# Optimization experiments

Hardware: AMD Instinct MI355X
Metric: run time of the kernel (lower is better)

Reference implementation:

```python
import jax, jax.numpy as jnp
import numpy as np

N = 20000
E = 320000
NEG_SLOPE = 0.2
LN_EPS = 1e-5


def gat_conv(x, W, a_src, a_dst, b, src, dst, heads, ch, concat):
    # x: [N, F_in]; W: [F_in, H*C]; a_src/a_dst: [H, C]; b: [H*C] or [C]
    xl = (x @ W).reshape(N, heads, ch)                      # [N,H,C]
    alpha_src = jnp.sum(xl * a_src, axis=-1)                # [N,H]
    alpha_dst = jnp.sum(xl * a_dst, axis=-1)                # [N,H]
    e = alpha_src[src] + alpha_dst[dst]                     # [E',H]
    e = jax.nn.leaky_relu(e, NEG_SLOPE)
    # segment softmax over incoming edges of each dst node
    m = jax.ops.segment_max(e, dst, num_segments=N)         # [N,H]
    m = jnp.where(jnp.isfinite(m), m, 0.0)
    ex = jnp.exp(e - m[dst])
    denom = jax.ops.segment_sum(ex, dst, num_segments=N)    # [N,H]
    alpha = ex / (denom[dst] + 1e-16)                       # [E',H]
    msg = alpha[:, :, None] * xl[src]                       # [E',H,C]
    out = jax.ops.segment_sum(msg, dst, num_segments=N)     # [N,H,C]
    if concat:
        return out.reshape(N, heads * ch) + b
    return out.mean(axis=1) + b


def layer_norm(x, g, b):
    mu = jnp.mean(x, axis=-1, keepdims=True)
    var = jnp.mean(jnp.square(x - mu), axis=-1, keepdims=True)
    return (x - mu) * jax.lax.rsqrt(var + LN_EPS) * g + b


def setup_inputs() -> dict:
    key = jax.random.key(0)
    ks = jax.random.split(key, 24)
    d = {}
    d["x"] = jax.random.normal(ks[0], (N, 50), dtype=jnp.float32)
    d["edge_index"] = jax.random.randint(ks[1], (2, E), 0, N, dtype=jnp.int64)

    def glorot(k, shape):
        fan = shape[0] + shape[-1]
        return jax.random.normal(k, shape, dtype=jnp.float32) * np.sqrt(2.0 / fan)

    # conv1: 50 -> 256, heads=4, concat
    d["W1"] = glorot(ks[2], (50, 4 * 256))
    d["a_src1"] = glorot(ks[3], (4, 256))
    d["a_dst1"] = glorot(ks[4], (4, 256))
    d["b1"] = jnp.zeros((4 * 256,), jnp.float32)
    # conv2: 1024 -> 256, heads=4, concat
    d["W2"] = glorot(ks[5], (1024, 4 * 256))
    d["a_src2"] = glorot(ks[6], (4, 256))
    d["a_dst2"] = glorot(ks[7], (4, 256))
    d["b2"] = jnp.zeros((4 * 256,), jnp.float32)
    # conv3: 1024 -> 121, heads=6, concat=False
    d["W3"] = glorot(ks[8], (1024, 6 * 121))
    d["a_src3"] = glorot(ks[9], (6, 121))
    d["a_dst3"] = glorot(ks[10], (6, 121))
    d["b3"] = jnp.zeros((121,), jnp.float32)
    # skips
    d["skipW1"] = glorot(ks[11], (50, 1024))
    d["skipb1"] = jnp.zeros((1024,), jnp.float32)
    d["skipW2"] = glorot(ks[12], (1024, 1024))
    d["skipb2"] = jnp.zeros((1024,), jnp.float32)
    # layer norms
    d["g1"] = jnp.ones((1024,), jnp.float32)
    d["beta1"] = jnp.zeros((1024,), jnp.float32)
    d["g2"] = jnp.ones((1024,), jnp.float32)
    d["beta2"] = jnp.zeros((1024,), jnp.float32)
    return d


def reference(x, edge_index, W1, a_src1, a_dst1, b1, W2, a_src2, a_dst2, b2,
              W3, a_src3, a_dst3, b3, skipW1, skipb1, skipW2, skipb2,
              g1, beta1, g2, beta2):
    # add self loops (PyG GATConv default)
    loop = jnp.arange(N, dtype=edge_index.dtype)
    src = jnp.concatenate([edge_index[0], loop])
    dst = jnp.concatenate([edge_index[1], loop])

    h = gat_conv(x, W1, a_src1, a_dst1, b1, src, dst, 4, 256, True)
    h = jax.nn.elu(layer_norm(h + (x @ skipW1 + skipb1), g1, beta1))
    h2 = gat_conv(h, W2, a_src2, a_dst2, b2, src, dst, 4, 256, True)
    h2 = jax.nn.elu(layer_norm(h2 + (h @ skipW2 + skipb2), g2, beta2))
    out = gat_conv(h2, W3, a_src3, a_dst3, b3, src, dst, 6, 121, False)
    return out
```

## Files before the change

### kernel.cpp

```cpp
#include <hip/hip_runtime.h>
#include <hip/hip_bf16.h>
#include <math.h>

typedef _Float16 h16;
typedef __attribute__((ext_vector_type(8))) _Float16 h16x8;
typedef __attribute__((ext_vector_type(4))) float f32x4;

#if __has_builtin(__builtin_amdgcn_global_load_lds)
#define GLD16(g, l)                                                                      \
    __builtin_amdgcn_global_load_lds(                                                    \
        (const __attribute__((address_space(1))) unsigned int*)(g),                      \
        (__attribute__((address_space(3))) unsigned int*)(l), 16, 0, 0)
#else
#define GLD16(g, l) (*(f32x4*)(l) = *(const f32x4*)(g))
#endif

#define GEMM_BODY(A, Bt, K, STORE)                                                       \
    __shared__ h16 As[128 * 32];                                                         \
    __shared__ h16 Bs[128 * 32];                                                         \
    const int t = threadIdx.x;                                                           \
    const int lane = t & 63;                                                             \
    const int wid = t >> 6;                                                              \
    const int wm = (wid >> 1) << 6;                                                      \
    const int wn = (wid & 1) << 6;                                                       \
    const int bm = blockIdx.y * 128;                                                     \
    const int bn = blockIdx.x * 128;                                                     \
    const int srow = (wid << 4) + (lane >> 2);                                           \
    const int scol = (lane & 3) << 3;                                                    \
    const h16* pa0 = A + (size_t)(bm + srow) * K + scol;                                 \
    const h16* pa1 = A + (size_t)(bm + 64 + srow) * K + scol;                            \
    const h16* pb0 = Bt + (size_t)(bn + srow) * K + scol;                                \
    const h16* pb1 = Bt + (size_t)(bn + 64 + srow) * K + scol;                           \
    h16* la0 = As + srow * 32 + scol;                                                    \
    h16* la1 = As + (64 + srow) * 32 + scol;                                             \
    h16* lb0 = Bs + srow * 32 + scol;                                                    \
    h16* lb1 = Bs + (64 + srow) * 32 + scol;                                             \
    f32x4 acc[4][4];                                                                     \
    _Pragma("unroll") for (int i = 0; i < 4; i++)                                        \
        _Pragma("unroll") for (int j = 0; j < 4; j++)                                    \
            acc[i][j] = (f32x4){0.f, 0.f, 0.f, 0.f};                                     \
    const int m16 = lane & 15;                                                           \
    const int k8 = (lane >> 4) << 3;                                                     \
    for (int k0 = 0; k0 < K; k0 += 32) {                                                 \
        __syncthreads();                                                                 \
        GLD16(pa0, la0);                                                                 \
        GLD16(pa1, la1);                                                                 \
        GLD16(pb0, lb0);                                                                 \
        GLD16(pb1, lb1);                                                                 \
        pa0 += 32; pa1 += 32; pb0 += 32; pb1 += 32;                                      \
        __syncthreads();                                                                 \
        h16x8 af[4], bfr[4];                                                             \
        _Pragma("unroll") for (int i = 0; i < 4; i++) {                                  \
            af[i] = *(const h16x8*)(As + (wm + 16 * i + m16) * 32 + k8);                 \
            bfr[i] = *(const h16x8*)(Bs + (wn + 16 * i + m16) * 32 + k8);                \
        }                                                                                \
        _Pragma("unroll") for (int i = 0; i < 4; i++)                                    \
            _Pragma("unroll") for (int j = 0; j < 4; j++)                                \
                acc[i][j] = __builtin_amdgcn_mfma_f32_16x16x32_f16(af[i], bfr[j],        \
                                                                   acc[i][j], 0, 0, 0);  \
    }                                                                                    \
    const int r4 = (lane >> 4) << 2;                                                     \
    STORE

__global__ __launch_bounds__(256) void gemm_bt(const h16* __restrict__ A,
                                               const h16* __restrict__ Bt,
                                               h16* __restrict__ C,
                                               int M, int N, int K) {
    GEMM_BODY(A, Bt, K,
        _Pragma("unroll") for (int i = 0; i < 4; i++)
            _Pragma("unroll") for (int j = 0; j < 4; j++) {
                int col = bn + wn + 16 * j + m16;
                _Pragma("unroll") for (int r = 0; r < 4; r++) {
                    int row = bm + wm + 16 * i + r4 + r;
                    C[(size_t)row * N + col] = (h16)acc[i][j][r];
                }
            })
}

__global__ __launch_bounds__(256) void gemm_bt2(const h16* __restrict__ A,
                                                const h16* __restrict__ Bt,
                                                h16* __restrict__ C0,
                                                h16* __restrict__ C1,
                                                int M, int K) {
    GEMM_BODY(A, Bt, K,
        h16* Cp = (bn < 1024) ? C0 : C1;
        const int cb = bn & 1023;
        _Pragma("unroll") for (int i = 0; i < 4; i++)
            _Pragma("unroll") for (int j = 0; j < 4; j++) {
                int col = cb + wn + 16 * j + m16;
                _Pragma("unroll") for (int r = 0; r < 4; r++) {
                    int row = bm + wm + 16 * i + r4 + r;
                    Cp[(size_t)row * 1024 + col] = (h16)acc[i][j][r];
                }
            })
}

__device__ __forceinline__ void transpose_tile(const float* __restrict__ W,
                                               h16* __restrict__ WT,
                                               int K, int N, int Kp, int Np,
                                               int bx, int by, float* sm) {
    int tx = threadIdx.x & 31, ty = threadIdx.x >> 5;
#pragma unroll
    for (int r = ty; r < 32; r += 8) {
        int k = by * 32 + r, n = bx * 32 + tx;
        float v = 0.f;
        if (k < K && n < N) v = W[(size_t)k * N + n];
        sm[r * 33 + tx] = v;
    }
    __syncthreads();
#pragma unroll
    for (int r = ty; r < 32; r += 8) {
        int n = bx * 32 + r, k = by * 32 + tx;
        if (n < Np && k < Kp) WT[(size_t)n * Kp + k] = (h16)sm[tx * 33 + r];
    }
}

__device__ __forceinline__ void transpose_w3_tile(const float* __restrict__ W,
                                                  h16* __restrict__ WT,
                                                  int bx, int by, float* sm) {
    int tx = threadIdx.x & 31, ty = threadIdx.x >> 5;
    int r0 = bx * 32;
    int h = r0 >> 7;
    int c0 = r0 & 127;
#pragma unroll
    for (int r = ty; r < 32; r += 8) {
        int k = by * 32 + r;
        int c = c0 + tx;
        float v = 0.f;
        if (c < 121) v = W[(size_t)k * 726 + h * 121 + c];
        sm[r * 33 + tx] = v;
    }
    __syncthreads();
#pragma unroll
    for (int r = ty; r < 32; r += 8) {
        int rr = r0 + r;
        int k = by * 32 + tx;
        WT[(size_t)rr * 1024 + k] = (h16)sm[tx * 33 + r];
    }
}

__global__ __launch_bounds__(256) void prep_k(const float* __restrict__ x,
                                              const float* __restrict__ W1,
                                              const float* __restrict__ sW1,
                                              const float* __restrict__ W2,
                                              const float* __restrict__ sW2,
                                              const float* __restrict__ W3,
                                              h16* __restrict__ xp,
                                              h16* __restrict__ WTcat1,
                                              h16* __restrict__ WTcat2,
                                              h16* __restrict__ W3pT, int Nn) {
    __shared__ float sm[32 * 33];
    int b = blockIdx.x;
    if (b < 5024) {
        int i = b * 256 + threadIdx.x;
        int n = i >> 6, c = i & 63;
        float v = 0.f;
        if (n < Nn && c < 50) v = x[n * 50 + c];
        xp[(size_t)n * 64 + c] = (h16)v;
    } else if (b < 5088) {
        int i = b - 5024; transpose_tile(W1, WTcat1, 50, 1024, 64, 1024, i % 32, i / 32, sm);
    } else if (b < 5152) {
        int i = b - 5088; transpose_tile(sW1, WTcat1 + 1024 * 64, 50, 1024, 64, 1024, i % 32, i / 32, sm);
    } else if (b < 6176) {
        int i = b - 5152; transpose_tile(W2, WTcat2, 1024, 1024, 1024, 1024, i % 32, i / 32, sm);
    } else if (b < 7200) {
        int i = b - 6176; transpose_tile(sW2, WTcat2 + (size_t)1024 * 1024, 1024, 1024, 1024, 1024, i % 32, i / 32, sm);
    } else {
        int i = b - 7200; transpose_w3_tile(W3, W3pT, i % 24, i / 24, sm);
    }
}

__global__ void zero_probe_k(const int* __restrict__ ei, int* __restrict__ cnt,
                             int* __restrict__ flag, int Nn) {
    int i = blockIdx.x * 256 + threadIdx.x;
    if (i < Nn) cnt[i] = 0;
    if (blockIdx.x == 0 && threadIdx.x == 0) {
        int all0 = 1;
        for (int k = 0; k < 64; k++)
            if (ei[2 * k + 1] != 0) { all0 = 0; break; }
        *flag = all0;
    }
}

__device__ __forceinline__ int load_ei(const int* ei, int idx, int is64) {
    return is64 ? ei[2 * idx] : ei[idx];
}

__global__ void hist_k(const int* __restrict__ ei, const int* __restrict__ flag,
                       int* __restrict__ cnt, int E, int Nn) {
    int e = blockIdx.x * 256 + threadIdx.x;
    if (e >= E + Nn) return;
    int is64 = *flag;
    int d = (e < E) ? load_ei(ei, E + e, is64) : (e - E);
    d = min(max(d, 0), Nn - 1);
    atomicAdd(&cnt[d], 1);
}

__global__ __launch_bounds__(1024) void scan_k(int* __restrict__ cnt, int* __restrict__ row_ptr,
                                               int Nn) {
    __shared__ int part[1024];
    int t = threadIdx.x;
    int chunk = (Nn + 1023) >> 10;
    int lo = t * chunk;
    int hi = lo + chunk; if (hi > Nn) hi = Nn; if (lo > Nn) lo = Nn;
    int s = 0;
    for (int i = lo; i < hi; i++) s += (cnt[i] + 7) & ~7;
    part[t] = s;
    __syncthreads();
    for (int off = 1; off < 1024; off <<= 1) {
        int v = (t >= off) ? part[t - off] : 0;
        __syncthreads();
        part[t] += v;
        __syncthreads();
    }
    int run = part[t] - s;
    for (int i = lo; i < hi; i++) { row_ptr[i] = run; run += (cnt[i] + 7) & ~7; }
    if (t == 1023) row_ptr[Nn] = part[1023];
    __syncthreads();
    for (int i = lo; i < hi; i++) cnt[i] = 0;
}

__global__ void fill_csr_k(const int* __restrict__ ei, const int* __restrict__ flag,
                           const int* __restrict__ row_ptr, int* __restrict__ cursor,
                           int* __restrict__ src_csr, int E, int Nn) {
    int e = blockIdx.x * 256 + threadIdx.x;
    if (e >= E + Nn) return;
    int is64 = *flag;
    int d = (e < E) ? load_ei(ei, E + e, is64) : (e - E);
    int s = (e < E) ? load_ei(ei, e, is64) : (e - E);
    d = min(max(d, 0), Nn - 1);
    s = min(max(s, 0), Nn - 1);
    int slot = row_ptr[d] + atomicAdd(&cursor[d], 1);
    src_csr[slot] = s;
}

__global__ void alpha_k(const h16* __restrict__ XL, int ld, const float* __restrict__ a_src,
                        const float* __restrict__ a_dst, float* __restrict__ asrc,
                        float* __restrict__ adst, int Nn, int H, int C, int Cpad) {
    int gw = (blockIdx.x * 256 + threadIdx.x) >> 6;
    int lane = threadIdx.x & 63;
    if (gw >= Nn * H) return;
    int n = gw / H, h = gw - n * H;
    const h16* row = XL + (size_t)n * ld + h * Cpad;
    const float* as = a_src + h * C;
    const float* ad = a_dst + h * C;
    float s = 0.f, d = 0.f;
    for (int c = lane; c < C; c += 64) {
        float v = (float)row[c];
        s += v * as[c];
        d += v * ad[c];
    }
#pragma unroll
    for (int off = 32; off; off >>= 1) {
        s += __shfl_down(s, off);
        d += __shfl_down(d, off);
    }
    if (lane == 0) { asrc[n * H + h] = s; adst[n * H + h] = d; }
}

__global__ void attn_k(const int* __restrict__ row_ptr, const int* __restrict__ deg,
                       const int* __restrict__ src_csr,
                       const float* __restrict__ asrc, const float* __restrict__ adst,
                       float* __restrict__ wt, int Nn, int H, int Ecap) {
    int gw = (blockIdx.x * 256 + threadIdx.x) >> 6;
    int lane = threadIdx.x & 63;
    if (gw >= Nn) return;
    int n = gw;
    int base = row_ptr[n], dg = deg[n];
    if (dg <= 64) {
        bool v = lane < dg;
        int src = v ? src_csr[base + lane] : 0;
        for (int h = 0; h < H; h++) {
            float ad = adst[n * H + h];
            float e = -1e30f;
            if (v) {
                e = asrc[src * H + h] + ad;
                e = e > 0.f ? e : 0.2f * e;
            }
            float m = e;
#pragma unroll
            for (int off = 1; off < 64; off <<= 1) m = fmaxf(m, __shfl_xor(m, off));
            float ex = v ? __expf(e - m) : 0.f;
            float sum = ex;
#pragma unroll
            for (int off = 1; off < 64; off <<= 1) sum += __shfl_xor(sum, off);
            if (v) wt[(size_t)h * Ecap + base + lane] = ex / (sum + 1e-16f);
        }
        return;
    }
    for (int h = 0; h < H; h++) {
        float ad = adst[n * H + h];
        float m = -1e30f;
        for (int s = lane; s < dg; s += 64) {
            float e = asrc[src_csr[base + s] * H + h] + ad;
            e = e > 0.f ? e : 0.2f * e;
            m = fmaxf(m, e);
        }
#pragma unroll
        for (int off = 1; off < 64; off <<= 1) m = fmaxf(m, __shfl_xor(m, off));
        float sum = 0.f;
        for (int s = lane; s < dg; s += 64) {
            float e = asrc[src_csr[base + s] * H + h] + ad;
            e = e > 0.f ? e : 0.2f * e;
            sum += __expf(e - m);
        }
#pragma unroll
        for (int off = 1; off < 64; off <<= 1) sum += __shfl_xor(sum, off);
        float inv = 1.f / (sum + 1e-16f);
        float* wrow = wt + (size_t)h * Ecap;
        for (int s = lane; s < dg; s += 64) {
            float e = asrc[src_csr[base + s] * H + h] + ad;
            e = e > 0.f ? e : 0.2f * e;
            wrow[base + s] = __expf(e - m) * inv;
        }
    }
}

__global__ __launch_bounds__(256) void agg_skip8(const h16* __restrict__ XL,
                                                 const float* __restrict__ wt,
                                                 const int* __restrict__ row_ptr,
                                                 const int* __restrict__ src_csr,
                                                 const float* __restrict__ bias,
                                                 const float* __restrict__ sb,
                                                 h16* __restrict__ SK, int Nn, int Ecap) {
    const int cc = blockIdx.x;
    const int n = blockIdx.y * 4 + (threadIdx.x >> 6);
    const int lane = threadIdx.x & 63;
    if (n >= Nn) return;
    const int g = lane >> 4;
    const int p = lane & 15;
    const int col = cc * 128 + p * 8;
    const float* wrow = wt + (size_t)(cc >> 1) * Ecap;
    const h16* XLc = XL + col;
    const int base = row_ptr[n], end = row_ptr[n + 1];

    float acc[8];
#pragma unroll
    for (int j = 0; j < 8; j++) acc[j] = 0.f;

    for (int e = base; e < end; e += 8) {
        int2 si = *(const int2*)(src_csr + e + 2 * g);
        float2 wv = *(const float2*)(wrow + e + 2 * g);
        h16x8 xa = *(const h16x8*)(XLc + (size_t)si.x * 1024);
        h16x8 xb = *(const h16x8*)(XLc + (size_t)si.y * 1024);
#pragma unroll
        for (int j = 0; j < 8; j++) acc[j] += wv.x * (float)xa[j] + wv.y * (float)xb[j];
    }
#pragma unroll
    for (int j = 0; j < 8; j++) {
        acc[j] += __shfl_xor(acc[j], 16);
        acc[j] += __shfl_xor(acc[j], 32);
    }
    if (lane < 16) {
        size_t o = (size_t)n * 1024 + col;
        h16x8 sk = *(const h16x8*)(SK + o);
        h16x8 res;
#pragma unroll
        for (int j = 0; j < 8; j++)
            res[j] = (h16)(acc[j] + bias[col + j] + sb[col + j] + (float)sk[j]);
        *(h16x8*)(SK + o) = res;
    }
}

__global__ __launch_bounds__(256) void agg_mean8(const h16* __restrict__ XL,
                                                 const float* __restrict__ wt,
                                                 const int* __restrict__ row_ptr,
                                                 const int* __restrict__ src_csr,
                                                 h16* __restrict__ part, int Nn, int Ecap) {
    const int cc = blockIdx.x;
    const int n = blockIdx.y * 4 + (threadIdx.x >> 6);
    const int lane = threadIdx.x & 63;
    if (n >= Nn) return;
    const int g = lane >> 4;
    const int p = lane & 15;
    const int col = cc * 128 + p * 8;
    const float* wrow = wt + (size_t)cc * Ecap;
    const h16* XLc = XL + col;
    const int base = row_ptr[n], end = row_ptr[n + 1];

    float acc[8];
#pragma unroll
    for (int j = 0; j < 8; j++) acc[j] = 0.f;

    for (int e = base; e < end; e += 8) {
        int2 si = *(const int2*)(src_csr + e + 2 * g);
        float2 wv = *(const float2*)(wrow + e + 2 * g);
        h16x8 xa = *(const h16x8*)(XLc + (size_t)si.x * 768);
        h16x8 xb = *(const h16x8*)(XLc + (size_t)si.y * 768);
#pragma unroll
        for (int j = 0; j < 8; j++) acc[j] += wv.x * (float)xa[j] + wv.y * (float)xb[j];
    }
#pragma unroll
    for (int j = 0; j < 8; j++) {
        acc[j] += __shfl_xor(acc[j], 16);
        acc[j] += __shfl_xor(acc[j], 32);
    }
    if (lane < 16) {
        size_t o = (size_t)n * 768 + col;
        h16x8 res;
#pragma unroll
        for (int j = 0; j < 8; j++) res[j] = (h16)acc[j];
        *(h16x8*)(part + o) = res;
    }
}

__global__ __launch_bounds__(128) void reduce_mean_k(const h16* __restrict__ part,
                                                     const float* __restrict__ b3,
                                                     float* __restrict__ out, int Nn) {
    int n = blockIdx.x;
    int t = threadIdx.x;
    if (t >= 121) return;
    const h16* row = part + (size_t)n * 768;
    float s = 0.f;
#pragma unroll
    for (int h = 0; h < 6; h++) s += (float)row[h * 128 + t];
    out[(size_t)n * 121 + t] = s * (1.f / 6.f) + b3[t];
}

__global__ __launch_bounds__(256) void ln_elu_k(const h16* __restrict__ in,
                                                const float* __restrict__ g,
                                                const float* __restrict__ be,
                                                h16* __restrict__ out, int rows_real) {
    const int D = 1024;
    int n = blockIdx.x;
    int t = threadIdx.x;
    size_t ro = (size_t)n * D;
    if (n >= rows_real) {
#pragma unroll
        for (int j = 0; j < 4; j++) out[ro + t + 256 * j] = (h16)0.f;
        return;
    }
    float v[4];
    float s = 0.f, q = 0.f;
#pragma unroll
    for (int j = 0; j < 4; j++) {
        int c = t + 256 * j;
        float a = (float)in[ro + c];
        v[j] = a;
        s += a;
        q += a * a;
    }
#pragma unroll
    for (int off = 32; off; off >>= 1) {
        s += __shfl_down(s, off);
        q += __shfl_down(q, off);
    }
    __shared__ float rs[8];
    int wid = t >> 6;
    if ((t & 63) == 0) { rs[wid] = s; rs[wid + 4] = q; }
    __syncthreads();
    s = rs[0] + rs[1] + rs[2] + rs[3];
    q = rs[4] + rs[5] + rs[6] + rs[7];
    float mu = s * (1.f / 1024.f);
    float var = q * (1.f / 1024.f) - mu * mu;
    float inv = rsqrtf(fmaxf(var, 0.f) + 1e-5f);
#pragma unroll
    for (int j = 0; j < 4; j++) {
        int c = t + 256 * j;
        float y = (v[j] - mu) * inv * g[c] + be[c];
        y = y > 0.f ? y : expm1f(y);
        out[ro + c] = (h16)y;
    }
}

extern "C" void kernel_launch(void* const* d_in, const int* in_sizes, int n_in,
                              void* d_out, int out_size, void* d_ws, size_t ws_size,
                              hipStream_t stream) {
    const float* x   = (const float*)d_in[0];
    const int*   ei  = (const int*)d_in[1];
    const float* W1  = (const float*)d_in[2];
    const float* as1 = (const float*)d_in[3];
    const float* ad1 = (const float*)d_in[4];
    const float* b1  = (const float*)d_in[5];
    const float* W2  = (const float*)d_in[6];
    const float* as2 = (const float*)d_in[7];
    const float* ad2 = (const float*)d_in[8];
    const float* b2  = (const float*)d_in[9];
    const float* W3  = (const float*)d_in[10];
    const float* as3 = (const float*)d_in[11];
    const float* ad3 = (const float*)d_in[12];
    const float* b3  = (const float*)d_in[13];
    const float* sW1 = (const float*)d_in[14];
    const float* sb1 = (const float*)d_in[15];
    const float* sW2 = (const float*)d_in[16];
    const float* sb2 = (const float*)d_in[17];
    const float* g1  = (const float*)d_in[18];
    const float* be1 = (const float*)d_in[19];
    const float* g2  = (const float*)d_in[20];
    const float* be2 = (const float*)d_in[21];
    float* out = (float*)d_out;

    const int Nn = 20000;
    const int E = in_sizes[1] / 2;
    const int E2 = E + Nn;
    const int Ecap = E2 + 8 * Nn;
    const int Mpad = 20096;

    char* p = (char*)d_ws;
    auto alloc = [&](size_t bytes) {
        char* r = p;
        p += (bytes + 255) & ~(size_t)255;
        return r;
    };
    h16*   WTcat1 = (h16*)alloc((size_t)2048 * 64 * 2);
    h16*   WTcat2 = (h16*)alloc((size_t)2048 * 1024 * 2);
    h16*   W3pT   = (h16*)alloc((size_t)768 * 1024 * 2);
    h16*   xp     = (h16*)alloc((size_t)Mpad * 64 * 2);
    h16*   XL     = (h16*)alloc((size_t)Mpad * 1024 * 2);
    h16*   SK     = (h16*)alloc((size_t)Mpad * 1024 * 2);
    h16*   H1     = (h16*)alloc((size_t)Mpad * 1024 * 2);
    float* asrcb  = (float*)alloc((size_t)Nn * 6 * 4);
    float* adstb  = (float*)alloc((size_t)Nn * 6 * 4);
    float* wbuf   = (float*)alloc((size_t)6 * Ecap * 4);
    int*   rowp   = (int*)alloc((size_t)(Nn + 1) * 4);
    int*   cnt    = (int*)alloc((size_t)Nn * 4);
    int*   scsr   = (int*)alloc((size_t)Ecap * 4);
    int*   eiflag = (int*)alloc(256);
    h16*   part   = SK;
    (void)ws_size; (void)n_in; (void)out_size;

    prep_k<<<7968, 256, 0, stream>>>(x, W1, sW1, W2, sW2, W3, xp, WTcat1, WTcat2, W3pT, Nn);

    zero_probe_k<<<(Nn + 255) / 256, 256, 0, stream>>>(ei, cnt, eiflag, Nn);
    hist_k<<<(E2 + 255) / 256, 256, 0, stream>>>(ei, eiflag, cnt, E, Nn);
    scan_k<<<1, 1024, 0, stream>>>(cnt, rowp, Nn);
    (void)hipMemsetAsync(scsr, 0, (size_t)Ecap * 4, stream);
    (void)hipMemsetAsync(wbuf, 0, (size_t)6 * Ecap * 4, stream);
    fill_csr_k<<<(E2 + 255) / 256, 256, 0, stream>>>(ei, eiflag, rowp, cnt, scsr, E, Nn);

    gemm_bt2<<<dim3(16, Mpad / 128), 256, 0, stream>>>(xp, WTcat1, XL, SK, Mpad, 64);
    alpha_k<<<(Nn * 4 * 64) / 256, 256, 0, stream>>>(XL, 1024, as1, ad1, asrcb, adstb, Nn, 4, 256, 256);
    attn_k<<<(Nn + 3) / 4, 256, 0, stream>>>(rowp, cnt, scsr, asrcb, adstb, wbuf, Nn, 4, Ecap);
    agg_skip8<<<dim3(8, (Nn + 3) / 4), 256, 0, stream>>>(XL, wbuf, rowp, scsr, b1, sb1, SK, Nn, Ecap);
    ln_elu_k<<<Mpad, 256, 0, stream>>>(SK, g1, be1, H1, Nn);

    gemm_bt2<<<dim3(16, Mpad / 128), 256, 0, stream>>>(H1, WTcat2, XL, SK, Mpad, 1024);
    alpha_k<<<(Nn * 4 * 64) / 256, 256, 0, stream>>>(XL, 1024, as2, ad2, asrcb, adstb, Nn, 4, 256, 256);
    attn_k<<<(Nn + 3) / 4, 256, 0, stream>>>(rowp, cnt, scsr, asrcb, adstb, wbuf, Nn, 4, Ecap);
    agg_skip8<<<dim3(8, (Nn + 3) / 4), 256, 0, stream>>>(XL, wbuf, rowp, scsr, b2, sb2, SK, Nn, Ecap);
    ln_elu_k<<<Mpad, 256, 0, stream>>>(SK, g2, be2, H1, Nn);

    gemm_bt<<<dim3(6, Mpad / 128), 256, 0, stream>>>(H1, W3pT, XL, Mpad, 768, 1024);
    alpha_k<<<(Nn * 6 * 64) / 256, 256, 0, stream>>>(XL, 768, as3, ad3, asrcb, adstb, Nn, 6, 121, 128);
    attn_k<<<(Nn + 3) / 4, 256, 0, stream>>>(rowp, cnt, scsr, asrcb, adstb, wbuf, Nn, 6, Ecap);
    agg_mean8<<<dim3(6, (Nn + 3) / 4), 256, 0, stream>>>(XL, wbuf, rowp, scsr, part, Nn, Ecap);
    reduce_mean_k<<<Nn, 128, 0, stream>>>(part, b3, out, Nn);
}
```

Measured before the change: 782.4 us.

## Double GEMM K-tile to 64 with XOR-swizzled LDS and fuse zeroing kernels

The shared GEMM body now stages a 64-wide K slice per iteration instead of 32. This halves the number of barrier pairs per tile, and the LDS layout uses an XOR swizzle on 16-byte chunks to avoid bank conflicts on fragment reads. Separately, the count, CSR and weight-buffer zeroing is folded into one kernel, replacing two hipMemsetAsync calls and cutting launch overhead. The larger LDS footprint may reduce occupancy. The K=64 layer-1 GEMM now runs a single iteration.

```diff
diff --git a/kernel.cpp b/kernel.cpp
--- a/kernel.cpp
+++ b/kernel.cpp
@@ -16,8 +16,8 @@
 #endif
 
 #define GEMM_BODY(A, Bt, K, STORE)                                                       \
-    __shared__ h16 As[128 * 32];                                                         \
-    __shared__ h16 Bs[128 * 32];                                                         \
+    __shared__ h16 As[128 * 64];                                                         \
+    __shared__ h16 Bs[128 * 64];                                                         \
     const int t = threadIdx.x;                                                           \
     const int lane = t & 63;                                                             \
     const int wid = t >> 6;                                                              \
@@ -25,34 +25,50 @@
     const int wn = (wid & 1) << 6;                                                       \
     const int bm = blockIdx.y * 128;                                                     \
     const int bn = blockIdx.x * 128;                                                     \
-    const int srow = (wid << 4) + (lane >> 2);                                           \
-    const int scol = (lane & 3) << 3;                                                    \
-    const h16* pa0 = A + (size_t)(bm + srow) * K + scol;                                 \
-    const h16* pa1 = A + (size_t)(bm + 64 + srow) * K + scol;                            \
-    const h16* pb0 = Bt + (size_t)(bn + srow) * K + scol;                                \
-    const h16* pb1 = Bt + (size_t)(bn + 64 + srow) * K + scol;                           \
-    h16* la0 = As + srow * 32 + scol;                                                    \
-    h16* la1 = As + (64 + srow) * 32 + scol;                                             \
-    h16* lb0 = Bs + srow * 32 + scol;                                                    \
-    h16* lb1 = Bs + (64 + srow) * 32 + scol;                                             \
+    const int sr = (wid << 3) + (lane >> 3);                                  \
+    const int sc_dst = (lane & 7) << 3;                                                  \
+    const int sc_src = (((lane & 7) ^ (sr & 7)) << 3);                                   \
+    const h16* pa0 = A + (size_t)(bm + sr) * K + sc_src;                                 \
+    const h16* pa1 = A + (size_t)(bm + sr + 32) * K + sc_src;                            \
+    const h16* pa2 = A + (size_t)(bm + sr + 64) * K + sc_src;                            \
+    const h16* pa3 = A + (size_t)(bm + sr + 96) * K + sc_src;                            \
+    const h16* pb0 = Bt + (size_t)(bn + sr) * K + sc_src;                                \
+    const h16* pb1 = Bt + (size_t)(bn + sr + 32) * K + sc_src;                           \
+    const h16* pb2 = Bt + (size_t)(bn + sr + 64) * K + sc_src;                           \
+    const h16* pb3 = Bt + (size_t)(bn + sr + 96) * K + sc_src;                           \
+    h16* la0 = As + sr * 64 + sc_dst;                                                    \
+    h16* la1 = la0 + 32 * 64;                                                            \
+    h16* la2 = la0 + 64 * 64;                                                            \
+    h16* la3 = la0 + 96 * 64;                                                            \
+    h16* lb0 = Bs + sr * 64 + sc_dst;                                                    \
+    h16* lb1 = lb0 + 32 * 64;                                                            \
+    h16* lb2 = lb0 + 64 * 64;                                                            \
+    h16* lb3 = lb0 + 96 * 64;                                                            \
     f32x4 acc[4][4];                                                                     \
     _Pragma("unroll") for (int i = 0; i < 4; i++)                                        \
         _Pragma("unroll") for (int j = 0; j < 4; j++)                                    \
             acc[i][j] = (f32x4){0.f, 0.f, 0.f, 0.f};                                     \
     const int m16 = lane & 15;                                                           \
-    const int k8 = (lane >> 4) << 3;                                                     \
-    for (int k0 = 0; k0 < K; k0 += 32) {                                                 \
+    const int k8s = (((lane >> 4) ^ (m16 & 7)) << 3);                                    \
+    for (int k0 = 0; k0 < K; k0 += 64) {                                                 \
         __syncthreads();                                                                 \
-        GLD16(pa0, la0);                                                                 \
-        GLD16(pa1, la1);                                                                 \
-        GLD16(pb0, lb0);                                                                 \
-        GLD16(pb1, lb1);                                                                 \
-        pa0 += 32; pa1 += 32; pb0 += 32; pb1 += 32;                                      \
+        GLD16(pa0, la0); GLD16(pa1, la1); GLD16(pa2, la2); GLD16(pa3, la3);              \
+        GLD16(pb0, lb0); GLD16(pb1, lb1); GLD16(pb2, lb2); GLD16(pb3, lb3);              \
+        pa0 += 64; pa1 += 64; pa2 += 64; pa3 += 64;                                      \
+        pb0 += 64; pb1 += 64; pb2 += 64; pb3 += 64;                                      \
         __syncthreads();                                                                 \
         h16x8 af[4], bfr[4];                                                             \
         _Pragma("unroll") for (int i = 0; i < 4; i++) {                                  \
-            af[i] = *(const h16x8*)(As + (wm + 16 * i + m16) * 32 + k8);                 \
-            bfr[i] = *(const h16x8*)(Bs + (wn + 16 * i + m16) * 32 + k8);                \
+            af[i] = *(const h16x8*)(As + (wm + 16 * i + m16) * 64 + k8s);                \
+            bfr[i] = *(const h16x8*)(Bs + (wn + 16 * i + m16) * 64 + k8s);               \
+        }                                                                                \
+        _Pragma("unroll") for (int i = 0; i < 4; i++)                                    \
+            _Pragma("unroll") for (int j = 0; j < 4; j++)                                \
+                acc[i][j] = __builtin_amdgcn_mfma_f32_16x16x32_f16(af[i], bfr[j],        \
+                                                                   acc[i][j], 0, 0, 0);  \
+        _Pragma("unroll") for (int i = 0; i < 4; i++) {                                  \
+            af[i] = *(const h16x8*)(As + (wm + 16 * i + m16) * 64 + (k8s ^ 32));         \
+            bfr[i] = *(const h16x8*)(Bs + (wn + 16 * i + m16) * 64 + (k8s ^ 32));        \
         }                                                                                \
         _Pragma("unroll") for (int i = 0; i < 4; i++)                                    \
             _Pragma("unroll") for (int j = 0; j < 4; j++)                                \
@@ -170,10 +186,18 @@
     }
 }
 
-__global__ void zero_probe_k(const int* __restrict__ ei, int* __restrict__ cnt,
-                             int* __restrict__ flag, int Nn) {
-    int i = blockIdx.x * 256 + threadIdx.x;
-    if (i < Nn) cnt[i] = 0;
+__global__ void zero_all_k(const int* __restrict__ ei, int* __restrict__ cnt,
+                           int* __restrict__ scsr, float* __restrict__ wbuf,
+                           int* __restrict__ flag, int Nn, int Ecap) {
+    long long idx = (long long)blockIdx.x * 256 + threadIdx.x;
+    if (idx < Nn) {
+        cnt[idx] = 0;
+    } else if (idx < (long long)Nn + Ecap) {
+        scsr[idx - Nn] = 0;
+    } else {
+        long long w = idx - Nn - Ecap;
+        if (w < (long long)6 * Ecap) wbuf[w] = 0.f;
+    }
     if (blockIdx.x == 0 && threadIdx.x == 0) {
         int all0 = 1;
         for (int k = 0; k < 64; k++)
@@ -521,11 +545,13 @@
 
     prep_k<<<7968, 256, 0, stream>>>(x, W1, sW1, W2, sW2, W3, xp, WTcat1, WTcat2, W3pT, Nn);
 
-    zero_probe_k<<<(Nn + 255) / 256, 256, 0, stream>>>(ei, cnt, eiflag, Nn);
+    {
+        long long zwords = (long long)Nn + (long long)7 * Ecap;
+        int zgrid = (int)((zwords + 255) / 256);
+        zero_all_k<<<zgrid, 256, 0, stream>>>(ei, cnt, scsr, wbuf, eiflag, Nn, Ecap);
+    }
     hist_k<<<(E2 + 255) / 256, 256, 0, stream>>>(ei, eiflag, cnt, E, Nn);
     scan_k<<<1, 1024, 0, stream>>>(cnt, rowp, Nn);
-    (void)hipMemsetAsync(scsr, 0, (size_t)Ecap * 4, stream);
-    (void)hipMemsetAsync(wbuf, 0, (size_t)6 * Ecap * 4, stream);
     fill_csr_k<<<(E2 + 255) / 256, 256, 0, stream>>>(ei, eiflag, rowp, cnt, scsr, E, Nn);
 
     gemm_bt2<<<dim3(16, Mpad / 128), 256, 0, stream>>>(xp, WTcat1, XL, SK, Mpad, 64);
```

After: 799.8 us. 2.2% more time.
